# Optimization experiments

Measured on AMD Instinct MI355X. Metric: run time of the kernel, lower is better.

The kernel has to match this reference:

```python
import jax, jax.numpy as jnp
import numpy as np

N_HOLES = 1
LENGTH = 16


def setup_inputs() -> dict:
    key = jax.random.key(0)
    k1, k2, k3 = jax.random.split(key, 3)
    B, C, H, W = 256, 3, 224, 224
    x = jax.random.normal(k1, (B, C, H, W), dtype=jnp.float32)
    cy = jax.random.randint(k2, (N_HOLES, B), 0, H, dtype=jnp.int32)
    cx = jax.random.randint(k3, (N_HOLES, B), 0, W, dtype=jnp.int32)
    return {"x": x, "cy": cy, "cx": cx}


def reference(x, cy, cx):
    # x: [B,C,H,W]; cy, cx: [n_holes, B] hole centers.
    B, C, H, W = x.shape
    half = LENGTH // 2
    ys = jnp.arange(H, dtype=jnp.int32)  # [H]
    xs = jnp.arange(W, dtype=jnp.int32)  # [W]
    # inside box: cy-half <= y < cy+half (clipping to image is implicit
    # since ys is in [0, H)). Shapes: [n_holes, B, H] and [n_holes, B, W].
    in_y = (ys[None, None, :] >= (cy - half)[:, :, None]) & (
        ys[None, None, :] < (cy + half)[:, :, None]
    )
    in_x = (xs[None, None, :] >= (cx - half)[:, :, None]) & (
        xs[None, None, :] < (cx + half)[:, :, None]
    )
    # hole coverage per pixel: any hole covering -> mask 0
    covered = jnp.any(in_y[:, :, :, None] & in_x[:, :, None, :], axis=0)  # [B,H,W]
    mask = jnp.where(covered[:, None, :, :], jnp.float32(0), jnp.float32(1))
    return x * mask
```

## Files before the change

### kernel.cpp

```cpp
#include <hip/hip_runtime.h>


typedef float floatx4 __attribute__((ext_vector_type(4)));

#define B_ 256
#define C_ 3
#define H_ 224
#define W_ 224
#define HALF 8
#define W4_ (W_ / 4)
#define PLANE4 (H_ * W4_)
#define BLOCKS_X (PLANE4 / 256)

__global__ __launch_bounds__(256) void cutout_kernel(
    const floatx4* __restrict__ x,
    const int* __restrict__ cy,
    const int* __restrict__ cx,
    floatx4* __restrict__ out) {
    const int plane = blockIdx.y;
    const int b = plane / C_;
    const int ip = blockIdx.x * 256 + threadIdx.x;

    const int y  = ip / W4_;
    const int x4 = ip - y * W4_;

    const long gidx = (long)plane * PLANE4 + ip;
    floatx4 v = __builtin_nontemporal_load(&x[gidx]);

    const int cyb = cy[b];
    const int cxb = cx[b];

    if (y >= cyb - HALF && y < cyb + HALF) {
        const int x0 = x4 * 4;
        const int lo = cxb - HALF;
        const int hi = cxb + HALF;
        v.x = (x0     >= lo && x0     < hi) ? 0.0f : v.x;
        v.y = (x0 + 1 >= lo && x0 + 1 < hi) ? 0.0f : v.y;
        v.z = (x0 + 2 >= lo && x0 + 2 < hi) ? 0.0f : v.z;
        v.w = (x0 + 3 >= lo && x0 + 3 < hi) ? 0.0f : v.w;
    }

    __builtin_nontemporal_store(v, &out[gidx]);
}

extern "C" void kernel_launch(void* const* d_in, const int* in_sizes, int n_in,
                              void* d_out, int out_size, void* d_ws, size_t ws_size,
                              hipStream_t stream) {
    const floatx4* x  = (const floatx4*)d_in[0];
    const int*     cy = (const int*)d_in[1];
    const int*     cx = (const int*)d_in[2];
    floatx4* out = (floatx4*)d_out;

    dim3 grid(BLOCKS_X, B_ * C_);
    cutout_kernel<<<grid, 256, 0, stream>>>(x, cy, cx, out);
}
```

Baseline: 250.9 us.

## Replace masked copy kernel with device memcpy plus small hole-zeroing kernel

```diff
diff --git a/kernel.cpp b/kernel.cpp
--- a/kernel.cpp
+++ b/kernel.cpp
@@ -1,56 +1,41 @@
 #include <hip/hip_runtime.h>
 
-
-typedef float floatx4 __attribute__((ext_vector_type(4)));
 
 #define B_ 256
 #define C_ 3
 #define H_ 224
 #define W_ 224
 #define HALF 8
-#define W4_ (W_ / 4)
-#define PLANE4 (H_ * W4_)
-#define BLOCKS_X (PLANE4 / 256)
 
-__global__ __launch_bounds__(256) void cutout_kernel(
-    const floatx4* __restrict__ x,
+__global__ __launch_bounds__(256) void hole_zero_kernel(
     const int* __restrict__ cy,
     const int* __restrict__ cx,
-    floatx4* __restrict__ out) {
-    const int plane = blockIdx.y;
-    const int b = plane / C_;
-    const int ip = blockIdx.x * 256 + threadIdx.x;
-
-    const int y  = ip / W4_;
-    const int x4 = ip - y * W4_;
-
-    const long gidx = (long)plane * PLANE4 + ip;
-    floatx4 v = __builtin_nontemporal_load(&x[gidx]);
-
+    float* __restrict__ out) {
+    const int b = blockIdx.x;
     const int cyb = cy[b];
     const int cxb = cx[b];
-
-    if (y >= cyb - HALF && y < cyb + HALF) {
-        const int x0 = x4 * 4;
-        const int lo = cxb - HALF;
-        const int hi = cxb + HALF;
-        v.x = (x0     >= lo && x0     < hi) ? 0.0f : v.x;
-        v.y = (x0 + 1 >= lo && x0 + 1 < hi) ? 0.0f : v.y;
-        v.z = (x0 + 2 >= lo && x0 + 2 < hi) ? 0.0f : v.z;
-        v.w = (x0 + 3 >= lo && x0 + 3 < hi) ? 0.0f : v.w;
+    const int ty = threadIdx.x >> 4;
+    const int tx = threadIdx.x & 15;
+    const int y = cyb - HALF + ty;
+    const int x = cxb - HALF + tx;
+    if ((unsigned)y < (unsigned)H_ && (unsigned)x < (unsigned)W_) {
+#pragma unroll
+        for (int c = 0; c < C_; ++c) {
+            const int idx = ((b * C_ + c) * H_ + y) * W_ + x;
+            out[idx] = 0.0f;
+        }
     }
-
-    __builtin_nontemporal_store(v, &out[gidx]);
 }
 
 extern "C" void kernel_launch(void* const* d_in, const int* in_sizes, int n_in,
                               void* d_out, int out_size, void* d_ws, size_t ws_size,
                               hipStream_t stream) {
-    const floatx4* x  = (const floatx4*)d_in[0];
-    const int*     cy = (const int*)d_in[1];
-    const int*     cx = (const int*)d_in[2];
-    floatx4* out = (floatx4*)d_out;
+    const void* x  = d_in[0];
+    const int*  cy = (const int*)d_in[1];
+    const int*  cx = (const int*)d_in[2];
 
-    dim3 grid(BLOCKS_X, B_ * C_);
-    cutout_kernel<<<grid, 256, 0, stream>>>(x, cy, cx, out);
+    const size_t bytes = (size_t)B_ * C_ * H_ * W_ * sizeof(float);
+    hipMemcpyAsync(d_out, x, bytes, hipMemcpyDeviceToDevice, stream);
+
+    hole_zero_kernel<<<dim3(B_), 256, 0, stream>>>(cy, cx, (float*)d_out);
 }
```

Result: slower. 261.8 us (+4.3%).
